# Kernel tuning notes

Hardware: AMD Instinct MI355X
Metric: run time of the kernel (lower is better)

Reference implementation:

```python
import jax, jax.numpy as jnp
import numpy as np

B, S, D, H = 2, 2048, 1024, 16
DK = D // H


def setup_inputs() -> dict:
    key = jax.random.key(0)
    ks = jax.random.split(key, 7)
    q = jax.random.normal(ks[0], (B, S, D), dtype=jnp.float32)
    k = jax.random.normal(ks[1], (B, S, D), dtype=jnp.float32)
    v = jax.random.normal(ks[2], (B, S, D), dtype=jnp.float32)
    # causal mask, broadcastable [B,1,S,S]; masked_fill where mask==0
    mask = jnp.broadcast_to(jnp.tril(jnp.ones((S, S), dtype=jnp.int32)), (B, 1, S, S))
    scale = 0.02
    Wq = jax.random.normal(ks[3], (D, D), dtype=jnp.float32) * scale
    Wk = jax.random.normal(ks[4], (D, D), dtype=jnp.float32) * scale
    Wv = jax.random.normal(ks[5], (D, D), dtype=jnp.float32) * scale
    Wo = jax.random.normal(ks[6], (D, D), dtype=jnp.float32) * scale
    return {"q": q, "k": k, "v": v, "mask": mask, "Wq": Wq, "Wk": Wk, "Wv": Wv, "Wo": Wo}


def reference(q, k, v, mask, Wq, Wk, Wv, Wo):
    # torch nn.Linear(bias=False): y = x @ W.T with W of shape [out, in]
    def proj(x, W):
        return (x @ W.T).reshape(B, S, H, DK).transpose(0, 2, 1, 3)  # [B,H,S,DK]

    Q = proj(q, Wq)
    K = proj(k, Wk)
    V = proj(v, Wv)
    inv_sqrt_dk = np.float32(1.0 / np.sqrt(DK))
    scores = jnp.einsum('bhqd,bhkd->bhqk', Q, K) * inv_sqrt_dk  # [B,H,S,S]
    scores = jnp.where(mask == 0, jnp.float32(-jnp.inf), scores)
    attn = jax.nn.softmax(scores, axis=-1)
    x = jnp.einsum('bhqk,bhkd->bhqd', attn, V)  # [B,H,S,DK]
    x = x.transpose(0, 2, 1, 3).reshape(B, S, D)
    return x @ Wo.T
```

## Files before the change

### kernel.cpp

```cpp
#include <hip/hip_runtime.h>

typedef __bf16 bf16x8 __attribute__((ext_vector_type(8)));
typedef __bf16 bf16x2 __attribute__((ext_vector_type(2)));
typedef float  f32x4  __attribute__((ext_vector_type(4)));

#define DEV static __device__ __forceinline__
#define VMCNT(n) asm volatile("s_waitcnt vmcnt(" #n ")" ::: "memory")
#define LGKM0()  asm volatile("s_waitcnt lgkmcnt(0)" ::: "memory")
#define SBAR()   __builtin_amdgcn_s_barrier()
#define SFENCE() __builtin_amdgcn_sched_barrier(0)


DEV ushort f2bf(float f) {
    return __builtin_bit_cast(ushort, (__bf16)f);
}
DEV uint pk2(float a, float b) {
    bf16x2 t; t[0] = (__bf16)a; t[1] = (__bf16)b;
    return __builtin_bit_cast(uint, t);
}

DEV void stage_swz(const ushort* g, int gstride, char* lds, int nchunks) {
    const int tid  = threadIdx.x;
    const int lane = tid & 63;
    const int wave = tid >> 6;
    for (int c0 = wave * 64; c0 < nchunks; c0 += 256) {
        int c   = c0 + lane;
        int row = c >> 3;
        int cc  = (c & 7) ^ (row & 7);
        const ushort* src = g + row * gstride + cc * 8;
        __builtin_amdgcn_global_load_lds((__attribute__((address_space(1))) void*)src,
                                         (__attribute__((address_space(3))) void*)(lds + c0 * 16),
                                         16, 0, 0);
    }
}

DEV bf16x8 ldfrag(const char* tile, int row, int kc) {
    int off = (row << 7) + ((kc ^ (row & 7)) << 4);
    return *(const bf16x8*)(tile + off);
}


struct CvtArgs { const float* s[7]; ushort* d[7]; int n[7]; };

__global__ void cvt_kernel(CvtArgs a) {
    const int y = blockIdx.y;
    const float* __restrict__ s = a.s[y];
    ushort* __restrict__ d = a.d[y];
    const int n = a.n[y];
    const int stride = gridDim.x * blockDim.x;
    for (int i = blockIdx.x * blockDim.x + threadIdx.x; i * 8 < n; i += stride) {
        const float4* p = (const float4*)(s + (size_t)i * 8);
        float4 x = p[0], yv = p[1];
        uint4 o;
        o.x = pk2(x.x,  x.y);
        o.y = pk2(x.z,  x.w);
        o.z = pk2(yv.x, yv.y);
        o.w = pk2(yv.z, yv.w);
        *(uint4*)(d + (size_t)i * 8) = o;
    }
}


constexpr int GN = 1024, GK = 1024;

template<typename EPI>
DEV void gemm_body(const ushort* __restrict__ A, const ushort* __restrict__ W,
                   char* smem, EPI epi) {
    const int tid  = threadIdx.x;
    const int lane = tid & 63;
    const int w    = tid >> 6;
    const int wr   = w >> 1, wc = w & 1;
    const int hi   = lane >> 4, lj = lane & 15;
    const int nb   = blockIdx.x & 7, mb = blockIdx.x >> 3;

    f32x4 acc[4][4];
#pragma unroll
    for (int mi = 0; mi < 4; mi++)
#pragma unroll
        for (int ni = 0; ni < 4; ni++) acc[mi][ni] = f32x4{0.f, 0.f, 0.f, 0.f};

    const ushort* Ag = A + (size_t)mb * 128 * GK;
    const ushort* Wg = W + (size_t)nb * 128 * GK;

    stage_swz(Ag, GK, smem, 1024);
    stage_swz(Wg, GK, smem + 32768, 1024);
    int cur = 0;
    for (int k0 = 0; k0 < GK; k0 += 64) {
        char* Ac = smem + (cur << 14);
        char* Wc = smem + 32768 + (cur << 14);
        if (k0 + 64 < GK) {
            stage_swz(Ag + k0 + 64, GK, smem + ((cur ^ 1) << 14), 1024);
            stage_swz(Wg + k0 + 64, GK, smem + 32768 + ((cur ^ 1) << 14), 1024);
            VMCNT(8);
        } else {
            VMCNT(0);
        }
        SBAR(); SFENCE();
#pragma unroll
        for (int kk = 0; kk < 2; ++kk) {
            bf16x8 a[4], b[4];
#pragma unroll
            for (int mi = 0; mi < 4; mi++) a[mi] = ldfrag(Ac, wr * 64 + mi * 16 + lj, kk * 4 + hi);
#pragma unroll
            for (int ni = 0; ni < 4; ni++) b[ni] = ldfrag(Wc, wc * 64 + ni * 16 + lj, kk * 4 + hi);
#pragma unroll
            for (int mi = 0; mi < 4; mi++)
#pragma unroll
                for (int ni = 0; ni < 4; ni++)
                    acc[mi][ni] = __builtin_amdgcn_mfma_f32_16x16x32_bf16(a[mi], b[ni], acc[mi][ni], 0, 0, 0);
        }
        LGKM0();
        SBAR(); SFENCE();
        cur ^= 1;
    }

#pragma unroll
    for (int mi = 0; mi < 4; mi++)
#pragma unroll
        for (int r = 0; r < 4; r++) {
            const int gm = mb * 128 + wr * 64 + mi * 16 + hi * 4 + r;
#pragma unroll
            for (int ni = 0; ni < 4; ni++) {
                const int gn = nb * 128 + wc * 64 + ni * 16 + lj;
                epi(gm, gn, acc[mi][ni][r]);
            }
        }
}

struct ProjArgs {
    const ushort* A[3]; const ushort* W[3]; ushort* O[3];
    float scale[3]; int mode[3];
};

__global__ __launch_bounds__(256) void gemm_proj(ProjArgs args) {
    __shared__ char smem[65536];
    const int z = blockIdx.z;
    const ushort* A = args.A[z];
    const ushort* W = args.W[z];
    ushort* Out = args.O[z];
    const float scale = args.scale[z];
    const int mode = args.mode[z];
    gemm_body(A, W, smem, [&](int gm, int gn, float v) {
        v *= scale;
        const int b_ = gm >> 11, s_ = gm & 2047;
        const int h_ = gn >> 6,  d_ = gn & 63;
        size_t off;
        if (mode == 0) off = (((size_t)b_ * 16 + h_) * 2048 + s_) * 64 + d_;
        else           off = (((size_t)b_ * 16 + h_) * 64 + d_) * 2048 + s_;
        Out[off] = f2bf(v);
    });
}

__global__ __launch_bounds__(256) void gemm_out(const ushort* __restrict__ A,
                                                const ushort* __restrict__ W,
                                                float* __restrict__ Out) {
    __shared__ char smem[65536];
    gemm_body(A, W, smem, [&](int gm, int gn, float v) {
        Out[(size_t)gm * GN + gn] = v;
    });
}


__global__ __launch_bounds__(256) void attn_kernel(const ushort* __restrict__ Qb,
                                                   const ushort* __restrict__ Kb,
                                                   const ushort* __restrict__ Vt,
                                                   ushort* __restrict__ Xb) {
    constexpr int S = 2048;
    __shared__ char smem[49152];
    const int tid = threadIdx.x, lane = tid & 63, w = tid >> 6;
    const int hi = lane >> 4, lj = lane & 15;
    char* Pw = smem + 32768 + w * 4096;
    const int bh = blockIdx.x;
    const int yraw = blockIdx.y;
    const int qt = (yraw < 8) ? 15 - yraw : yraw - 8;
    const int q0 = qt * 128;
    const int q0w = q0 + w * 32;

    const ushort* Qg = Qb + (size_t)bh * S * 64;
    const ushort* Kg = Kb + (size_t)bh * S * 64;
    const ushort* Vg = Vt + (size_t)bh * 64 * S;

    bf16x8 qf[2][2];
#pragma unroll
    for (int mi = 0; mi < 2; mi++)
#pragma unroll
        for (int kk = 0; kk < 2; kk++)
            qf[mi][kk] = *(const bf16x8*)(Qg + (size_t)(q0w + mi * 16 + lj) * 64 + kk * 32 + hi * 8);

    f32x4 o[2][4];
    float m_run[2] = { -1e30f, -1e30f }, l_run[2] = { 0.f, 0.f };
#pragma unroll
    for (int mi = 0; mi < 2; mi++)
#pragma unroll
        for (int nd = 0; nd < 4; nd++) o[mi][nd] = f32x4{0.f, 0.f, 0.f, 0.f};

    const int nt = qt * 2 + 2;
    stage_swz(Kg, 64, smem, 512);
    stage_swz(Vg, S, smem + 16384, 512);
    int cur = 0;

    for (int t = 0; t < nt; ++t) {
        char* Kc = smem + (cur << 13);
        char* Vc = smem + 16384 + (cur << 13);
        if (t + 1 < nt) {
            stage_swz(Kg + (size_t)(t + 1) * 64 * 64, 64, smem + ((cur ^ 1) << 13), 512);
            stage_swz(Vg + (t + 1) * 64, S, smem + 16384 + ((cur ^ 1) << 13), 512);
            VMCNT(4);
        } else {
            VMCNT(0);
        }
        SBAR(); SFENCE();

        if (t * 64 <= q0w + 31) {
            f32x4 sc[2][4];
#pragma unroll
            for (int mi = 0; mi < 2; mi++)
#pragma unroll
                for (int ni = 0; ni < 4; ni++) sc[mi][ni] = f32x4{0.f, 0.f, 0.f, 0.f};
            __builtin_amdgcn_s_setprio(1);
#pragma unroll
            for (int kk = 0; kk < 2; ++kk) {
                bf16x8 kf[4];
#pragma unroll
                for (int ni = 0; ni < 4; ni++) kf[ni] = ldfrag(Kc, ni * 16 + lj, kk * 4 + hi);
#pragma unroll
                for (int mi = 0; mi < 2; mi++)
#pragma unroll
                    for (int ni = 0; ni < 4; ni++)
                        sc[mi][ni] = __builtin_amdgcn_mfma_f32_16x16x32_bf16(kf[ni], qf[mi][kk], sc[mi][ni], 0, 0, 0);
            }
            __builtin_amdgcn_s_setprio(0);

            const bool diag = (t * 64 + 63 > q0w);
#pragma unroll
            for (int mi = 0; mi < 2; mi++) {
                const int q = q0w + mi * 16 + lj;
                if (diag) {
#pragma unroll
                    for (int ni = 0; ni < 4; ni++)
#pragma unroll
                        for (int r = 0; r < 4; r++)
                            if (t * 64 + ni * 16 + hi * 4 + r > q) sc[mi][ni][r] = -1e30f;
                }
                float mx = -1e30f;
#pragma unroll
                for (int ni = 0; ni < 4; ni++)
#pragma unroll
                    for (int r = 0; r < 4; r++) mx = fmaxf(mx, sc[mi][ni][r]);
                mx = fmaxf(mx, __shfl_xor(mx, 16));
                mx = fmaxf(mx, __shfl_xor(mx, 32));
                const float mo = m_run[mi];
                const bool defer = __all(mx <= mo + 8.f);
                float mn, rs;
                if (defer) { mn = mo; rs = 1.f; }
                else { mn = fmaxf(mo, mx); rs = __builtin_exp2f(mo - mn); m_run[mi] = mn; }
                float ps = 0.f;
                const int row = mi * 16 + lj;
#pragma unroll
                for (int ni = 0; ni < 4; ni++) {
                    float p0 = __builtin_exp2f(sc[mi][ni][0] - mn);
                    float p1 = __builtin_exp2f(sc[mi][ni][1] - mn);
                    float p2 = __builtin_exp2f(sc[mi][ni][2] - mn);
                    float p3 = __builtin_exp2f(sc[mi][ni][3] - mn);
                    ps += (p0 + p1) + (p2 + p3);
                    uint2 pv; pv.x = pk2(p0, p1); pv.y = pk2(p2, p3);
                    const int c = ni * 2 + (hi >> 1);
                    *(uint2*)(Pw + row * 128 + ((c ^ (row & 7)) << 4) + ((hi & 1) << 3)) = pv;
                }
                ps += __shfl_xor(ps, 16);
                ps += __shfl_xor(ps, 32);
                if (defer) {
                    l_run[mi] += ps;
                } else {
                    l_run[mi] = l_run[mi] * rs + ps;
#pragma unroll
                    for (int r = 0; r < 4; r++) {
                        float rr = __shfl(rs, (lane & 48) | (hi * 4 + r));
#pragma unroll
                        for (int nd = 0; nd < 4; nd++) o[mi][nd][r] *= rr;
                    }
                }
            }

            LGKM0(); SFENCE();

            __builtin_amdgcn_s_setprio(1);
#pragma unroll
            for (int kk = 0; kk < 2; ++kk) {
                bf16x8 pa[2], bv[4];
#pragma unroll
                for (int mi = 0; mi < 2; mi++) pa[mi] = ldfrag(Pw, mi * 16 + lj, kk * 4 + hi);
#pragma unroll
                for (int nd = 0; nd < 4; nd++) bv[nd] = ldfrag(Vc, nd * 16 + lj, kk * 4 + hi);
#pragma unroll
                for (int mi = 0; mi < 2; mi++)
#pragma unroll
                    for (int nd = 0; nd < 4; nd++)
                        o[mi][nd] = __builtin_amdgcn_mfma_f32_16x16x32_bf16(pa[mi], bv[nd], o[mi][nd], 0, 0, 0);
            }
            __builtin_amdgcn_s_setprio(0);
        }

        LGKM0();
        SBAR(); SFENCE();
        cur ^= 1;
    }

    const int b_ = bh >> 4, h_ = bh & 15;
#pragma unroll
    for (int mi = 0; mi < 2; mi++)
#pragma unroll
        for (int r = 0; r < 4; r++) {
            float lv = __shfl(l_run[mi], (lane & 48) | (hi * 4 + r));
            float inv = 1.f / lv;
            const int srow = q0w + mi * 16 + hi * 4 + r;
#pragma unroll
            for (int nd = 0; nd < 4; nd++)
                Xb[((size_t)b_ * S + srow) * 1024 + h_ * 64 + nd * 16 + lj] =
                    f2bf(o[mi][nd][r] * inv);
        }
}


extern "C" void kernel_launch(void* const* d_in, const int* in_sizes, int n_in,
                              void* d_out, int out_size, void* d_ws, size_t ws_size,
                              hipStream_t stream) {
    (void)in_sizes; (void)n_in; (void)out_size; (void)ws_size;
    const float* q  = (const float*)d_in[0];
    const float* k  = (const float*)d_in[1];
    const float* v  = (const float*)d_in[2];
    const float* Wq = (const float*)d_in[4];
    const float* Wk = (const float*)d_in[5];
    const float* Wv = (const float*)d_in[6];
    const float* Wo = (const float*)d_in[7];

    char* ws = (char*)d_ws;
    const size_t MB = (size_t)1 << 20;
    ushort* Qb  = (ushort*)(ws + 0 * MB);
    ushort* Kb  = (ushort*)(ws + 8 * MB);
    ushort* Vtb = (ushort*)(ws + 16 * MB);
    ushort* Xb  = (ushort*)(ws + 24 * MB);
    ushort* qb  = (ushort*)(ws + 32 * MB);
    ushort* kb  = (ushort*)(ws + 40 * MB);
    ushort* vb  = (ushort*)(ws + 48 * MB);
    ushort* Wqb = (ushort*)(ws + 56 * MB);
    ushort* Wkb = (ushort*)(ws + 58 * MB);
    ushort* Wvb = (ushort*)(ws + 60 * MB);
    ushort* Wob = (ushort*)(ws + 62 * MB);

    CvtArgs c;
    c.s[0] = q;  c.s[1] = k;  c.s[2] = v;  c.s[3] = Wq;  c.s[4] = Wk;  c.s[5] = Wv;  c.s[6] = Wo;
    c.d[0] = qb; c.d[1] = kb; c.d[2] = vb; c.d[3] = Wqb; c.d[4] = Wkb; c.d[5] = Wvb; c.d[6] = Wob;
    c.n[0] = c.n[1] = c.n[2] = 4 * 1024 * 1024;
    c.n[3] = c.n[4] = c.n[5] = c.n[6] = 1024 * 1024;
    cvt_kernel<<<dim3(1024, 7), 256, 0, stream>>>(c);

    ProjArgs p;
    p.A[0] = qb;  p.A[1] = kb;  p.A[2] = vb;
    p.W[0] = Wqb; p.W[1] = Wkb; p.W[2] = Wvb;
    p.O[0] = Qb;  p.O[1] = Kb;  p.O[2] = Vtb;
    p.scale[0] = 0.125f * 1.44269504088896f;
    p.scale[1] = 1.0f; p.scale[2] = 1.0f;
    p.mode[0] = 0; p.mode[1] = 0; p.mode[2] = 1;
    gemm_proj<<<dim3(256, 1, 3), 256, 0, stream>>>(p);

    attn_kernel<<<dim3(32, 16), 256, 0, stream>>>(Qb, Kb, Vtb, Xb);

    gemm_out<<<256, 256, 0, stream>>>(Xb, Wob, (float*)d_out);
}
```

Measured before the change: 262.0 us.

## Split long causal attention rows across two blocks and single-buffer GEMM LDS

The attention kernel now splits the eight longest query tiles into two key-range halves, each processed by its own block. Each half writes unnormalized partial outputs plus row max and sum to workspace, and a new merge kernel combines them. This targets load imbalance in the causal grid, at the cost of an extra launch and fp32 partial traffic. The GEMMs also drop double-buffered LDS staging for a single buffer with syncthreads and add occupancy hints for three blocks per CU, trading load/compute overlap for occupancy.

New measurement: 255.9 us. -2.3%, faster.

```diff
diff --git a/kernel.cpp b/kernel.cpp
--- a/kernel.cpp
+++ b/kernel.cpp
@@ -17,6 +17,15 @@
 DEV uint pk2(float a, float b) {
     bf16x2 t; t[0] = (__bf16)a; t[1] = (__bf16)b;
     return __builtin_bit_cast(uint, t);
+}
+
+DEV float redmax4(float x) {
+    x = fmaxf(x, __shfl_xor(x, 16));
+    return fmaxf(x, __shfl_xor(x, 32));
+}
+DEV float redsum4(float x) {
+    x += __shfl_xor(x, 16);
+    return x + __shfl_xor(x, 32);
 }
 
 DEV void stage_swz(const ushort* g, int gstride, char* lds, int nchunks) {
@@ -82,36 +91,24 @@
     const ushort* Ag = A + (size_t)mb * 128 * GK;
     const ushort* Wg = W + (size_t)nb * 128 * GK;
 
-    stage_swz(Ag, GK, smem, 1024);
-    stage_swz(Wg, GK, smem + 32768, 1024);
-    int cur = 0;
     for (int k0 = 0; k0 < GK; k0 += 64) {
-        char* Ac = smem + (cur << 14);
-        char* Wc = smem + 32768 + (cur << 14);
-        if (k0 + 64 < GK) {
-            stage_swz(Ag + k0 + 64, GK, smem + ((cur ^ 1) << 14), 1024);
-            stage_swz(Wg + k0 + 64, GK, smem + 32768 + ((cur ^ 1) << 14), 1024);
-            VMCNT(8);
-        } else {
-            VMCNT(0);
-        }
-        SBAR(); SFENCE();
+        __syncthreads();
+        stage_swz(Ag + k0, GK, smem, 1024);
+        stage_swz(Wg + k0, GK, smem + 16384, 1024);
+        __syncthreads();
 #pragma unroll
         for (int kk = 0; kk < 2; ++kk) {
             bf16x8 a[4], b[4];
 #pragma unroll
-            for (int mi = 0; mi < 4; mi++) a[mi] = ldfrag(Ac, wr * 64 + mi * 16 + lj, kk * 4 + hi);
-#pragma unroll
-            for (int ni = 0; ni < 4; ni++) b[ni] = ldfrag(Wc, wc * 64 + ni * 16 + lj, kk * 4 + hi);
+            for (int mi = 0; mi < 4; mi++) a[mi] = ldfrag(smem, wr * 64 + mi * 16 + lj, kk * 4 + hi);
+#pragma unroll
+            for (int ni = 0; ni < 4; ni++) b[ni] = ldfrag(smem + 16384, wc * 64 + ni * 16 + lj, kk * 4 + hi);
 #pragma unroll
             for (int mi = 0; mi < 4; mi++)
 #pragma unroll
                 for (int ni = 0; ni < 4; ni++)
                     acc[mi][ni] = __builtin_amdgcn_mfma_f32_16x16x32_bf16(a[mi], b[ni], acc[mi][ni], 0, 0, 0);
         }
-        LGKM0();
-        SBAR(); SFENCE();
-        cur ^= 1;
     }
 
 #pragma unroll
@@ -132,8 +129,8 @@
     float scale[3]; int mode[3];
 };
 
-__global__ __launch_bounds__(256) void gemm_proj(ProjArgs args) {
-    __shared__ char smem[65536];
+__global__ __launch_bounds__(256, 3) void gemm_proj(ProjArgs args) {
+    __shared__ char smem[32768];
     const int z = blockIdx.z;
     const ushort* A = args.A[z];
     const ushort* W = args.W[z];
@@ -151,28 +148,40 @@
     });
 }
 
-__global__ __launch_bounds__(256) void gemm_out(const ushort* __restrict__ A,
-                                                const ushort* __restrict__ W,
-                                                float* __restrict__ Out) {
-    __shared__ char smem[65536];
+__global__ __launch_bounds__(256, 3) void gemm_out(const ushort* __restrict__ A,
+                                                   const ushort* __restrict__ W,
+                                                   float* __restrict__ Out) {
+    __shared__ char smem[32768];
     gemm_body(A, W, smem, [&](int gm, int gn, float v) {
         Out[(size_t)gm * GN + gn] = v;
     });
 }
 
 
-__global__ __launch_bounds__(256) void attn_kernel(const ushort* __restrict__ Qb,
-                                                   const ushort* __restrict__ Kb,
-                                                   const ushort* __restrict__ Vt,
-                                                   ushort* __restrict__ Xb) {
+__global__ __launch_bounds__(256, 3) void attn_kernel(const ushort* __restrict__ Qb,
+                                                      const ushort* __restrict__ Kb,
+                                                      const ushort* __restrict__ Vt,
+                                                      ushort* __restrict__ Xb,
+                                                      float* __restrict__ Opart,
+                                                      float* __restrict__ Mlp) {
     constexpr int S = 2048;
     __shared__ char smem[49152];
     const int tid = threadIdx.x, lane = tid & 63, w = tid >> 6;
     const int hi = lane >> 4, lj = lane & 15;
     char* Pw = smem + 32768 + w * 4096;
     const int bh = blockIdx.x;
-    const int yraw = blockIdx.y;
-    const int qt = (yraw < 8) ? 15 - yraw : yraw - 8;
+    const int y = blockIdx.y;
+
+    int qt, kts, kte, half;
+    bool partial;
+    if (y < 16) {
+        qt = 15 - (y >> 1); half = y & 1; partial = true;
+        if (half == 0) { kts = 0; kte = qt + 1; }
+        else           { kts = qt + 1; kte = 2 * qt + 2; }
+    } else {
+        qt = 23 - y; half = 0; partial = false;
+        kts = 0; kte = 2 * qt + 2;
+    }
     const int q0 = qt * 128;
     const int q0w = q0 + w * 32;
 
@@ -194,15 +203,14 @@
 #pragma unroll
         for (int nd = 0; nd < 4; nd++) o[mi][nd] = f32x4{0.f, 0.f, 0.f, 0.f};
 
-    const int nt = qt * 2 + 2;
-    stage_swz(Kg, 64, smem, 512);
-    stage_swz(Vg, S, smem + 16384, 512);
+    stage_swz(Kg + (size_t)kts * 64 * 64, 64, smem, 512);
+    stage_swz(Vg + kts * 64, S, smem + 16384, 512);
     int cur = 0;
 
-    for (int t = 0; t < nt; ++t) {
+    for (int t = kts; t < kte; ++t) {
         char* Kc = smem + (cur << 13);
         char* Vc = smem + 16384 + (cur << 13);
-        if (t + 1 < nt) {
+        if (t + 1 < kte) {
             stage_swz(Kg + (size_t)(t + 1) * 64 * 64, 64, smem + ((cur ^ 1) << 13), 512);
             stage_swz(Vg + (t + 1) * 64, S, smem + 16384 + ((cur ^ 1) << 13), 512);
             VMCNT(4);
@@ -247,8 +255,7 @@
                 for (int ni = 0; ni < 4; ni++)
 #pragma unroll
                     for (int r = 0; r < 4; r++) mx = fmaxf(mx, sc[mi][ni][r]);
-                mx = fmaxf(mx, __shfl_xor(mx, 16));
-                mx = fmaxf(mx, __shfl_xor(mx, 32));
+                mx = redmax4(mx);
                 const float mo = m_run[mi];
                 const bool defer = __all(mx <= mo + 8.f);
                 float mn, rs;
@@ -267,8 +274,7 @@
                     const int c = ni * 2 + (hi >> 1);
                     *(uint2*)(Pw + row * 128 + ((c ^ (row & 7)) << 4) + ((hi & 1) << 3)) = pv;
                 }
-                ps += __shfl_xor(ps, 16);
-                ps += __shfl_xor(ps, 32);
+                ps = redsum4(ps);
                 if (defer) {
                     l_run[mi] += ps;
                 } else {
@@ -306,19 +312,74 @@
         cur ^= 1;
     }
 
+    if (partial) {
+        const int pidx = (((bh << 3) + (qt - 8)) << 1) + half;
+        float* Op = Opart + (size_t)pidx * 8192;
+        float* Ml = Mlp   + (size_t)pidx * 256;
+#pragma unroll
+        for (int mi = 0; mi < 2; mi++)
+#pragma unroll
+            for (int r = 0; r < 4; r++) {
+                const int row = w * 32 + mi * 16 + hi * 4 + r;
+#pragma unroll
+                for (int nd = 0; nd < 4; nd++)
+                    Op[row * 64 + nd * 16 + lj] = o[mi][nd][r];
+            }
+        if (hi == 0) {
+#pragma unroll
+            for (int mi = 0; mi < 2; mi++) {
+                const int row = w * 32 + mi * 16 + lj;
+                Ml[row * 2 + 0] = m_run[mi];
+                Ml[row * 2 + 1] = l_run[mi];
+            }
+        }
+    } else {
+        const int b_ = bh >> 4, h_ = bh & 15;
+#pragma unroll
+        for (int mi = 0; mi < 2; mi++)
+#pragma unroll
+            for (int r = 0; r < 4; r++) {
+                float lv = __shfl(l_run[mi], (lane & 48) | (hi * 4 + r));
+                float inv = 1.f / lv;
+                const int srow = q0w + mi * 16 + hi * 4 + r;
+#pragma unroll
+                for (int nd = 0; nd < 4; nd++)
+                    Xb[((size_t)b_ * S + srow) * 1024 + h_ * 64 + nd * 16 + lj] =
+                        f2bf(o[mi][nd][r] * inv);
+            }
+    }
+}
+
+
+__global__ __launch_bounds__(256) void attn_merge(const float* __restrict__ Op,
+                                                  const float* __restrict__ Ml,
+                                                  ushort* __restrict__ Xb) {
+    const int bh = blockIdx.x;
+    const int qt = 8 + blockIdx.y;
+    const int tid = threadIdx.x;
+    const int row = tid >> 1;
+    const int c0 = (tid & 1) * 32;
+    const int sbase = (((bh << 3) + (qt - 8)) << 1);
+    const float* o0 = Op + (size_t)(sbase + 0) * 8192 + row * 64 + c0;
+    const float* o1 = Op + (size_t)(sbase + 1) * 8192 + row * 64 + c0;
+    const float* ml0 = Ml + (size_t)(sbase + 0) * 256 + row * 2;
+    const float* ml1 = Ml + (size_t)(sbase + 1) * 256 + row * 2;
+    const float m0 = ml0[0], l0 = ml0[1];
+    const float m1 = ml1[0], l1 = ml1[1];
+    const float m = fmaxf(m0, m1);
+    const float a0 = __builtin_exp2f(m0 - m), a1 = __builtin_exp2f(m1 - m);
+    const float inv = 1.f / (l0 * a0 + l1 * a1);
     const int b_ = bh >> 4, h_ = bh & 15;
-#pragma unroll
-    for (int mi = 0; mi < 2; mi++)
-#pragma unroll
-        for (int r = 0; r < 4; r++) {
-            float lv = __shfl(l_run[mi], (lane & 48) | (hi * 4 + r));
-            float inv = 1.f / lv;
-            const int srow = q0w + mi * 16 + hi * 4 + r;
-#pragma unroll
-            for (int nd = 0; nd < 4; nd++)
-                Xb[((size_t)b_ * S + srow) * 1024 + h_ * 64 + nd * 16 + lj] =
-                    f2bf(o[mi][nd][r] * inv);
-        }
+    ushort* dst = Xb + ((size_t)b_ * 2048 + qt * 128 + row) * 1024 + h_ * 64 + c0;
+#pragma unroll
+    for (int c = 0; c < 32; c += 4) {
+        float4 x = *(const float4*)(o0 + c);
+        float4 y = *(const float4*)(o1 + c);
+        uint2 pv;
+        pv.x = pk2((x.x * a0 + y.x * a1) * inv, (x.y * a0 + y.y * a1) * inv);
+        pv.y = pk2((x.z * a0 + y.z * a1) * inv, (x.w * a0 + y.w * a1) * inv);
+        *(uint2*)(dst + c) = pv;
+    }
 }
 
 
@@ -347,6 +408,8 @@
     ushort* Wkb = (ushort*)(ws + 58 * MB);
     ushort* Wvb = (ushort*)(ws + 60 * MB);
     ushort* Wob = (ushort*)(ws + 62 * MB);
+    float*  Opart = (float*)(ws + 32 * MB);
+    float*  Mlp   = (float*)(ws + 48 * MB);
 
     CvtArgs c;
     c.s[0] = q;  c.s[1] = k;  c.s[2] = v;  c.s[3] = Wq;  c.s[4] = Wk;  c.s[5] = Wv;  c.s[6] = Wo;
@@ -364,7 +427,8 @@
     p.mode[0] = 0; p.mode[1] = 0; p.mode[2] = 1;
     gemm_proj<<<dim3(256, 1, 3), 256, 0, stream>>>(p);
 
-    attn_kernel<<<dim3(32, 16), 256, 0, stream>>>(Qb, Kb, Vtb, Xb);
+    attn_kernel<<<dim3(32, 24), 256, 0, stream>>>(Qb, Kb, Vtb, Xb, Opart, Mlp);
+    attn_merge<<<dim3(32, 8), 256, 0, stream>>>(Opart, Mlp, Xb);
 
     gemm_out<<<256, 256, 0, stream>>>(Xb, Wob, (float*)d_out);
 }
```
